# Performance work log

Hardware: AMD Instinct MI355X
Metric: run time of the kernel (lower is better)

Reference implementation:

```python
import jax, jax.numpy as jnp
import numpy as np

NU = 60000   # num_users
NI = 40000   # num_items
N = NU + NI  # num_nodes
E = 2000000  # num_edges
F = 128      # feat_dim (user_feat_dim == item_feat_dim)
H = 128      # hidden_dim


def setup_inputs() -> dict:
    key = jax.random.key(0)
    ks = jax.random.split(key, 14)
    s = 0.05
    inp = {
        "x": jax.random.normal(ks[0], (N, F), jnp.float32),
        "edge_index": jax.random.randint(ks[1], (2, E), 0, N, dtype=jnp.int32),
        "node_type": jnp.concatenate([jnp.zeros(NU, jnp.int32), jnp.ones(NI, jnp.int32)]),
        # input projections (Linear stores weight as (out, in))
        "w_user": s * jax.random.normal(ks[2], (H, F), jnp.float32),
        "b_user": jnp.zeros((H,), jnp.float32),
        "w_item": s * jax.random.normal(ks[3], (H, F), jnp.float32),
        "b_item": jnp.zeros((H,), jnp.float32),
        # SAGEConv layer 0: lin_l (aggregated neighbors, with bias), lin_r (root, no bias)
        "w_l0": s * jax.random.normal(ks[4], (H, H), jnp.float32),
        "b_l0": s * jax.random.normal(ks[5], (H,), jnp.float32),
        "w_r0": s * jax.random.normal(ks[6], (H, H), jnp.float32),
        # SAGEConv layer 1
        "w_l1": s * jax.random.normal(ks[7], (H, H), jnp.float32),
        "b_l1": s * jax.random.normal(ks[8], (H,), jnp.float32),
        "w_r1": s * jax.random.normal(ks[9], (H, H), jnp.float32),
    }
    return inp


def _sage_conv(h, src, dst, w_l, b_l, w_r):
    # gather source features, max-aggregate onto destinations (PyG aggr='max')
    msg = h[src]                                          # [E, H]
    agg = jax.ops.segment_max(msg, dst, num_segments=N)   # [N, H], -inf where no in-edges
    agg = jnp.where(jnp.isneginf(agg), 0.0, agg)          # PyG fills empty segments with 0
    return agg @ w_l.T + b_l + h @ w_r.T


def reference(x, edge_index, node_type, w_user, b_user, w_item, b_item,
              w_l0, b_l0, w_r0, w_l1, b_l1, w_r1):
    # node_type is sorted: first NU rows are users, rest are items
    src, dst = edge_index[0], edge_index[1]
    user_h = x[:NU] @ w_user.T + b_user                   # [NU, H]
    item_h = x[NU:] @ w_item.T + b_item                   # [NI, H]
    h = jnp.concatenate([user_h, item_h], axis=0)         # [N, H]
    # layer 0 with residual (dims match) then ReLU; dropout is identity in eval
    h = h + _sage_conv(h, src, dst, w_l0, b_l0, w_r0)
    h = jax.nn.relu(h)
    # layer 1 with residual (no activation after last layer)
    h = h + _sage_conv(h, src, dst, w_l1, b_l1, w_r1)
    return (h[:NU], h[NU:])
```

## Files before the change

kernel.cpp:

```cpp
#include <hip/hip_runtime.h>

#define NUSR 60000
#define NITM 40000
#define NN   100000
#define EE   2000000
#define HD   128

#define BW   512
#define NB   196
#define EPB  8192

using bf16x8   = __attribute__((ext_vector_type(8))) short;
using f32x4    = __attribute__((ext_vector_type(4))) float;
using ushort4t = __attribute__((ext_vector_type(4))) unsigned short;
using ushort2t = __attribute__((ext_vector_type(2))) unsigned short;
using ushort8t = __attribute__((ext_vector_type(8))) unsigned short;
using uint4t   = __attribute__((ext_vector_type(4))) unsigned int;

__device__ __forceinline__ unsigned short f2bf(float f) {
    unsigned int u = __float_as_uint(f);
    u += 0x7FFFu + ((u >> 16) & 1u);
    return (unsigned short)(u >> 16);
}
__device__ __forceinline__ float bf2f(unsigned short s) {
    return __uint_as_float(((unsigned int)s) << 16);
}
__device__ __forceinline__ unsigned short keyof(unsigned short b) {
    return (b & 0x8000u) ? (unsigned short)~b : (unsigned short)(b | 0x8000u);
}
__device__ __forceinline__ unsigned unkey32(unsigned k) {
    unsigned negsel = (~k & 0x80008000u) >> 15;
    return k ^ (0x80008000u | (negsel * 0x7FFFu));
}
__device__ __forceinline__ int swz(int row, int col) {
    return row * HD + (col ^ ((row & 7) << 3));
}
__device__ __forceinline__ ushort8t pkmax8(ushort8t a, ushort8t b) {
    return __builtin_elementwise_max(a, b);
}

__global__ __launch_bounds__(256) void bhist_k(const int* __restrict__ dst,
                                               int* __restrict__ bcnt) {
    __shared__ int h[NB];
    int t = threadIdx.x;
    if (t < NB) h[t] = 0;
    __syncthreads();
    int e0 = blockIdx.x * EPB;
    #pragma unroll 4
    for (int i = t; i < EPB; i += 256) {
        int e = e0 + i;
        if (e < EE) atomicAdd(&h[dst[e] >> 9], 1);
    }
    __syncthreads();
    if (t < NB && h[t]) atomicAdd(&bcnt[t], h[t]);
}

__global__ void bscan_k(const int* __restrict__ bcnt, int* __restrict__ bbase,
                        int* __restrict__ bcur, int* __restrict__ off) {
    __shared__ int s[256];
    int t = threadIdx.x;
    int v = (t < NB) ? bcnt[t] : 0;
    s[t] = v;
    __syncthreads();
    for (int d = 1; d < 256; d <<= 1) {
        int a = (t >= d) ? s[t - d] : 0;
        __syncthreads();
        s[t] += a;
        __syncthreads();
    }
    if (t < NB) { bbase[t] = s[t] - v; bcur[t] = s[t] - v; }
    if (t == NB - 1) { bbase[NB] = s[t]; off[NN] = EE; }
}

__global__ __launch_bounds__(256) void bscatter_k(const int* __restrict__ src,
                                                  const int* __restrict__ dst,
                                                  int* __restrict__ bcur,
                                                  unsigned int* __restrict__ bedge) {
    __shared__ int h[NB], base[NB];
    int t = threadIdx.x;
    if (t < NB) h[t] = 0;
    __syncthreads();
    int e0 = blockIdx.x * EPB;
    #pragma unroll 4
    for (int i = t; i < EPB; i += 256) {
        int e = e0 + i;
        if (e < EE) atomicAdd(&h[dst[e] >> 9], 1);
    }
    __syncthreads();
    if (t < NB) {
        int c = h[t];
        base[t] = c ? atomicAdd(&bcur[t], c) : 0;
        h[t] = 0;
    }
    __syncthreads();
    #pragma unroll 4
    for (int i = t; i < EPB; i += 256) {
        int e = e0 + i;
        if (e < EE) {
            int d = dst[e];
            int b = d >> 9;
            int p = base[b] + atomicAdd(&h[b], 1);
            bedge[p] = ((unsigned)(d - (b << 9)) << 17) | (unsigned)src[e];
        }
    }
}

__global__ __launch_bounds__(512) void bcsr_k(const unsigned int* __restrict__ bedge,
                                              const int* __restrict__ bbase,
                                              int* __restrict__ off,
                                              int* __restrict__ csr) {
    __shared__ int cnt[BW], cur[BW], sc[BW];
    int b = blockIdx.x, t = threadIdx.x;
    int n0 = b * BW;
    int nloc = min(BW, NN - n0);
    cnt[t] = 0;
    __syncthreads();
    int e0 = bbase[b], e1 = bbase[b + 1];
    for (int e = e0 + t; e < e1; e += 512)
        atomicAdd(&cnt[bedge[e] >> 17], 1);
    __syncthreads();
    int v = cnt[t];
    sc[t] = v;
    __syncthreads();
    for (int d = 1; d < BW; d <<= 1) {
        int a = (t >= d) ? sc[t - d] : 0;
        __syncthreads();
        sc[t] += a;
        __syncthreads();
    }
    int excl = sc[t] - v;
    if (t < nloc) { off[n0 + t] = e0 + excl; cur[t] = e0 + excl; }
    __syncthreads();
    for (int e = e0 + t; e < e1; e += 512) {
        unsigned ed = bedge[e];
        int p = atomicAdd(&cur[ed >> 17], 1);
        csr[p] = (int)(ed & 0x1FFFFu);
    }
}

__global__ void cvt6_k(const float* __restrict__ a0, const float* __restrict__ a1,
                       const float* __restrict__ a2, const float* __restrict__ a3,
                       const float* __restrict__ a4, const float* __restrict__ a5,
                       unsigned short* __restrict__ out) {
    int i = blockIdx.x * 256 + threadIdx.x;
    const float* s;
    switch (i >> 14) {
        case 0: s = a0; break; case 1: s = a1; break; case 2: s = a2; break;
        case 3: s = a3; break; case 4: s = a4; break; default: s = a5; break;
    }
    out[i] = f2bf(s[i & 16383]);
}

__global__ __launch_bounds__(256) void proj_mfma_k(
    const float* __restrict__ x, const unsigned short* __restrict__ wb,
    const float* __restrict__ bias, unsigned short* __restrict__ hkey,
    int row_base, int nrows) {
    __shared__ unsigned short lw[HD * HD];
    int tid = threadIdx.x;
    #pragma unroll
    for (int it = 0; it < 16; ++it) {
        int flat = (it * 256 + tid) * 4;
        int row = flat >> 7, col = flat & 127;
        *(ushort4t*)&lw[swz(row, col)] = *(const ushort4t*)(wb + flat);
    }
    __syncthreads();
    int lane = tid & 63, w = tid >> 6;
    int l15 = lane & 15, l4 = lane >> 4;
    int m0 = blockIdx.x * 128 + w * 32;
    f32x4 acc[2][8] = {};
    #pragma unroll
    for (int kb = 0; kb < 4; ++kb) {
        bf16x8 a[2];
        #pragma unroll
        for (int rt = 0; rt < 2; ++rt) {
            int r = m0 + rt * 16 + l15;
            if (r >= nrows) r = nrows - 1;
            const float* ap = x + (size_t)(row_base + r) * HD + kb * 32 + l4 * 8;
            f32x4 v0 = *(const f32x4*)ap;
            f32x4 v1 = *(const f32x4*)(ap + 4);
            bf16x8 f;
            #pragma unroll
            for (int j = 0; j < 4; ++j) { f[j] = (short)f2bf(v0[j]); f[j + 4] = (short)f2bf(v1[j]); }
            a[rt] = f;
        }
        #pragma unroll
        for (int ct = 0; ct < 8; ++ct) {
            bf16x8 b = *(const bf16x8*)&lw[swz(ct * 16 + l15, kb * 32 + l4 * 8)];
            acc[0][ct] = __builtin_amdgcn_mfma_f32_16x16x32_bf16(a[0], b, acc[0][ct], 0, 0, 0);
            acc[1][ct] = __builtin_amdgcn_mfma_f32_16x16x32_bf16(a[1], b, acc[1][ct], 0, 0, 0);
        }
    }
    __syncthreads();
    #pragma unroll
    for (int ct = 0; ct < 8; ++ct) {
        int col = ct * 16 + l15;
        float bv = bias[col];
        #pragma unroll
        for (int rt = 0; rt < 2; ++rt)
            #pragma unroll
            for (int j = 0; j < 4; ++j) {
                int lrow = w * 32 + rt * 16 + l4 * 4 + j;
                lw[lrow * HD + ((col + ((lrow & 15) << 3)) & 127)] =
                    keyof(f2bf(acc[rt][ct][j] + bv));
            }
    }
    __syncthreads();
    int row = tid >> 1, cb = (tid & 1) * 64;
    int r = blockIdx.x * 128 + row;
    if (r < nrows) {
        int sof = (row & 15) << 3;
        #pragma unroll
        for (int gg = 0; gg < 8; ++gg) {
            uint4t v = *(const uint4t*)&lw[row * HD + ((cb + gg * 8 + sof) & 127)];
            *(uint4t*)(hkey + (size_t)(row_base + r) * HD + cb + gg * 8) = v;
        }
    }
}

__global__ __launch_bounds__(256) void agg_key_k(
    const uint4t* __restrict__ hkey4,
    const int* __restrict__ off, const int* __restrict__ csr,
    uint4t* __restrict__ agg4) {
    int node = (blockIdx.x * 256 + threadIdx.x) >> 6;
    int lane = threadIdx.x & 63;
    if (node >= NN) return;
    int s0 = off[node], s1 = off[node + 1];
    int deg = s1 - s0;
    int q = lane >> 4, l16 = lane & 15;
    ushort8t m = {0, 0, 0, 0, 0, 0, 0, 0};
    int cval = (lane < deg) ? csr[s0 + lane] : 0;
    int nslots = deg < 64 ? deg : 64;
    #pragma unroll
    for (int u = 0; u < 16; ++u) {
        int idx = u * 4 + q;
        int r = __shfl(cval, idx, 64);
        if (idx < nslots) {
            uint4t v = hkey4[(size_t)r * 16 + l16];
            m = pkmax8(m, *(ushort8t*)&v);
        }
    }
    for (int base = s0 + 64; base < s1; base += 32) {
        #pragma unroll
        for (int u = 0; u < 8; ++u) {
            int jj = base + u * 4 + q;
            if (jj < s1) {
                int r = csr[jj];
                uint4t v = hkey4[(size_t)r * 16 + l16];
                m = pkmax8(m, *(ushort8t*)&v);
            }
        }
    }
    uint4t mu = *(uint4t*)&m;
    #pragma unroll
    for (int c = 0; c < 4; ++c) {
        unsigned a = mu[c];
        unsigned b = (unsigned)__shfl_xor((int)a, 16, 64);
        ushort2t pa = *(ushort2t*)&a, pb = *(ushort2t*)&b;
        pa = __builtin_elementwise_max(pa, pb);
        a = *(unsigned*)&pa;
        b = (unsigned)__shfl_xor((int)a, 32, 64);
        pb = *(ushort2t*)&b;
        pa = __builtin_elementwise_max(pa, pb);
        mu[c] = *(unsigned*)&pa;
    }
    if (q == 0) {
        uint4t outv = {0, 0, 0, 0};
        if (deg > 0) {
            #pragma unroll
            for (int c = 0; c < 4; ++c) outv[c] = unkey32(mu[c]);
        }
        agg4[(size_t)node * 16 + l16] = outv;
    }
}

__global__ __launch_bounds__(512) void combine_mfma_k(
    const unsigned short* __restrict__ hkey, const unsigned short* __restrict__ aggb,
    const unsigned short* __restrict__ wlb, const float* __restrict__ bl,
    const unsigned short* __restrict__ wrb,
    unsigned short* __restrict__ hkey_out, float* __restrict__ fout, int relu) {
    __shared__ unsigned short lw[2][HD * HD];
    int tid = threadIdx.x;
    #pragma unroll
    for (int it = 0; it < 8; ++it) {
        int flat = (it * 512 + tid) * 4;
        int row = flat >> 7, col = flat & 127;
        *(ushort4t*)&lw[0][swz(row, col)] = *(const ushort4t*)(wlb + flat);
        *(ushort4t*)&lw[1][swz(row, col)] = *(const ushort4t*)(wrb + flat);
    }
    __syncthreads();
    int lane = tid & 63, w = tid >> 6;
    int l15 = lane & 15, l4 = lane >> 4;
    int m0 = blockIdx.x * 256 + w * 32;
    const uint4t* hk4 = (const uint4t*)hkey;
    f32x4 acc[2][8] = {};
    #pragma unroll
    for (int kb = 0; kb < 4; ++kb) {
        bf16x8 a1[2], a2[2];
        #pragma unroll
        for (int rt = 0; rt < 2; ++rt) {
            int r = m0 + rt * 16 + l15;
            if (r >= NN) r = NN - 1;
            size_t o = (size_t)r * HD + kb * 32 + l4 * 8;
            a1[rt] = *(const bf16x8*)(aggb + o);
            uint4t aw = hk4[(size_t)r * 16 + kb * 4 + l4];
            bf16x8 f;
            #pragma unroll
            for (int u = 0; u < 4; ++u) {
                unsigned d = unkey32(aw[u]);
                f[2 * u]     = (short)(d & 0xFFFFu);
                f[2 * u + 1] = (short)(d >> 16);
            }
            a2[rt] = f;
        }
        #pragma unroll
        for (int ct = 0; ct < 8; ++ct) {
            bf16x8 b1 = *(const bf16x8*)&lw[0][swz(ct * 16 + l15, kb * 32 + l4 * 8)];
            bf16x8 b2 = *(const bf16x8*)&lw[1][swz(ct * 16 + l15, kb * 32 + l4 * 8)];
            acc[0][ct] = __builtin_amdgcn_mfma_f32_16x16x32_bf16(a1[0], b1, acc[0][ct], 0, 0, 0);
            acc[0][ct] = __builtin_amdgcn_mfma_f32_16x16x32_bf16(a2[0], b2, acc[0][ct], 0, 0, 0);
            acc[1][ct] = __builtin_amdgcn_mfma_f32_16x16x32_bf16(a1[1], b1, acc[1][ct], 0, 0, 0);
            acc[1][ct] = __builtin_amdgcn_mfma_f32_16x16x32_bf16(a2[1], b2, acc[1][ct], 0, 0, 0);
        }
    }
    __syncthreads();
    float* cs = (float*)lw;
    for (int p = 0; p < 2; ++p) {
        if ((w >> 2) == p) {
            #pragma unroll
            for (int ct = 0; ct < 8; ++ct)
                #pragma unroll
                for (int rt = 0; rt < 2; ++rt)
                    #pragma unroll
                    for (int j = 0; j < 4; ++j) {
                        int lrow = (w & 3) * 32 + rt * 16 + l4 * 4 + j;
                        int col = ct * 16 + l15;
                        cs[lrow * HD + ((col + lrow * 4) & 127)] = acc[rt][ct][j];
                    }
        }
        __syncthreads();
        int lrow = tid >> 2, cq = (tid & 3) * 32;
        int r = blockIdx.x * 256 + p * 128 + lrow;
        if (r < NN) {
            const float* crow = cs + lrow * HD;
            int rot = lrow * 4;
            #pragma unroll
            for (int gg = 0; gg < 4; ++gg) {
                int c0 = cq + gg * 8;
                uint4t res = *(const uint4t*)(hkey + (size_t)r * HD + c0);
                f32x4 cv0 = *(const f32x4*)&crow[(c0 + rot) & 127];
                f32x4 cv1 = *(const f32x4*)&crow[(c0 + 4 + rot) & 127];
                f32x4 bv0 = *(const f32x4*)(bl + c0);
                f32x4 bv1 = *(const f32x4*)(bl + c0 + 4);
                float v[8];
                #pragma unroll
                for (int u = 0; u < 4; ++u) {
                    unsigned d = unkey32(res[u]);
                    float c_lo = (u < 2) ? cv0[u * 2]     : cv1[(u - 2) * 2];
                    float c_hi = (u < 2) ? cv0[u * 2 + 1] : cv1[(u - 2) * 2 + 1];
                    float b_lo = (u < 2) ? bv0[u * 2]     : bv1[(u - 2) * 2];
                    float b_hi = (u < 2) ? bv0[u * 2 + 1] : bv1[(u - 2) * 2 + 1];
                    v[2 * u]     = c_lo + b_lo + bf2f((unsigned short)(d & 0xFFFFu));
                    v[2 * u + 1] = c_hi + b_hi + bf2f((unsigned short)(d >> 16));
                }
                if (relu) {
                    #pragma unroll
                    for (int u = 0; u < 8; ++u) v[u] = fmaxf(v[u], 0.0f);
                }
                if (fout) {
                    f32x4 o0 = {v[0], v[1], v[2], v[3]};
                    f32x4 o1 = {v[4], v[5], v[6], v[7]};
                    *(f32x4*)(fout + (size_t)r * HD + c0) = o0;
                    *(f32x4*)(fout + (size_t)r * HD + c0 + 4) = o1;
                } else {
                    uint4t ov;
                    #pragma unroll
                    for (int u = 0; u < 4; ++u)
                        ov[u] = (unsigned)keyof(f2bf(v[2 * u]))
                              | ((unsigned)keyof(f2bf(v[2 * u + 1])) << 16);
                    *(uint4t*)(hkey_out + (size_t)r * HD + c0) = ov;
                }
            }
        }
        __syncthreads();
    }
}

extern "C" void kernel_launch(void* const* d_in, const int* in_sizes, int n_in,
                              void* d_out, int out_size, void* d_ws, size_t ws_size,
                              hipStream_t stream) {
    const float* x      = (const float*)d_in[0];
    const int*   ei     = (const int*)d_in[1];
    const float* w_user = (const float*)d_in[3];
    const float* b_user = (const float*)d_in[4];
    const float* w_item = (const float*)d_in[5];
    const float* b_item = (const float*)d_in[6];
    const float* w_l0   = (const float*)d_in[7];
    const float* b_l0   = (const float*)d_in[8];
    const float* w_r0   = (const float*)d_in[9];
    const float* w_l1   = (const float*)d_in[10];
    const float* b_l1   = (const float*)d_in[11];
    const float* w_r1   = (const float*)d_in[12];

    const int* e_src = ei;
    const int* e_dst = ei + EE;

    char* ws = (char*)d_ws;
    size_t cur_off = 0;
    auto carve = [&](size_t bytes) {
        void* p = ws + cur_off;
        cur_off = (cur_off + bytes + 255) & ~(size_t)255;
        return p;
    };
    unsigned short* hkey0 = (unsigned short*)carve((size_t)NN * HD * 2);
    unsigned short* hkey1 = (unsigned short*)carve((size_t)NN * HD * 2);
    unsigned short* aggb  = (unsigned short*)carve((size_t)NN * HD * 2);
    unsigned short* wb    = (unsigned short*)carve((size_t)6 * HD * HD * 2);
    int*      off   = (int*)carve((size_t)(NN + 1) * 4);
    int*      csr   = (int*)carve((size_t)EE * 4);
    unsigned* bedge = (unsigned*)carve((size_t)EE * 4);
    int*      bcnt  = (int*)carve((NB + 1) * 4);
    int*      bbase = (int*)carve((NB + 1) * 4);
    int*      bcur  = (int*)carve((NB + 1) * 4);
    (void)ws_size;

    hipMemsetAsync(bcnt, 0, (size_t)NB * 4, stream);
    int nbB = (EE + EPB - 1) / EPB;
    bhist_k<<<nbB, 256, 0, stream>>>(e_dst, bcnt);
    bscan_k<<<1, 256, 0, stream>>>(bcnt, bbase, bcur, off);
    bscatter_k<<<nbB, 256, 0, stream>>>(e_src, e_dst, bcur, bedge);
    bcsr_k<<<NB, 512, 0, stream>>>(bedge, bbase, off, csr);

    cvt6_k<<<(6 * HD * HD) / 256, 256, 0, stream>>>(w_user, w_item, w_l0, w_r0, w_l1, w_r1, wb);

    proj_mfma_k<<<(NUSR + 127) / 128, 256, 0, stream>>>(x, wb,         b_user, hkey0, 0,    NUSR);
    proj_mfma_k<<<(NITM + 127) / 128, 256, 0, stream>>>(x, wb + 16384, b_item, hkey0, NUSR, NITM);

    agg_key_k<<<NN / 4, 256, 0, stream>>>((const uint4t*)hkey0, off, csr, (uint4t*)aggb);
    combine_mfma_k<<<(NN + 255) / 256, 512, 0, stream>>>(
        hkey0, aggb, wb + 2 * 16384, b_l0, wb + 3 * 16384, hkey1, nullptr, 1);

    agg_key_k<<<NN / 4, 256, 0, stream>>>((const uint4t*)hkey1, off, csr, (uint4t*)aggb);
    combine_mfma_k<<<(NN + 255) / 256, 512, 0, stream>>>(
        hkey1, aggb, wb + 4 * 16384, b_l1, wb + 5 * 16384, nullptr, (float*)d_out, 0);
}
```

Measured before the change: 314.3 us.

## Pre-pack MFMA weight fragments, fold residual into W_r, drop LDS weight staging

```diff
diff --git a/kernel.cpp b/kernel.cpp
--- a/kernel.cpp
+++ b/kernel.cpp
@@ -31,9 +31,6 @@
 __device__ __forceinline__ unsigned unkey32(unsigned k) {
     unsigned negsel = (~k & 0x80008000u) >> 15;
     return k ^ (0x80008000u | (negsel * 0x7FFFu));
-}
-__device__ __forceinline__ int swz(int row, int col) {
-    return row * HD + (col ^ ((row & 7) << 3));
 }
 __device__ __forceinline__ ushort8t pkmax8(ushort8t a, ushort8t b) {
     return __builtin_elementwise_max(a, b);
@@ -138,32 +135,38 @@
     }
 }
 
-__global__ void cvt6_k(const float* __restrict__ a0, const float* __restrict__ a1,
-                       const float* __restrict__ a2, const float* __restrict__ a3,
-                       const float* __restrict__ a4, const float* __restrict__ a5,
-                       unsigned short* __restrict__ out) {
-    int i = blockIdx.x * 256 + threadIdx.x;
+__global__ void pack6_k(const float* __restrict__ a0, const float* __restrict__ a1,
+                        const float* __restrict__ a2, const float* __restrict__ a3,
+                        const float* __restrict__ a4, const float* __restrict__ a5,
+                        unsigned short* __restrict__ wp) {
+    int g = blockIdx.x * 256 + threadIdx.x;
+    int m = g >> 11, rem = g & 2047;
+    int kb = rem >> 9, rem2 = rem & 511;
+    int ct = rem2 >> 6, lane = rem2 & 63;
+    int l15 = lane & 15, l4 = lane >> 4;
     const float* s;
-    switch (i >> 14) {
+    switch (m) {
         case 0: s = a0; break; case 1: s = a1; break; case 2: s = a2; break;
         case 3: s = a3; break; case 4: s = a4; break; default: s = a5; break;
     }
-    out[i] = f2bf(s[i & 16383]);
+    int n = ct * 16 + l15, k0 = kb * 32 + l4 * 8;
+    int addI = (m == 3 || m == 5);
+    ushort8t o;
+    #pragma unroll
+    for (int j = 0; j < 8; ++j) {
+        float v = s[n * HD + k0 + j];
+        if (addI && n == (k0 + j)) v += 1.0f;
+        o[j] = f2bf(v);
+    }
+    *(ushort8t*)&wp[(size_t)g * 8] = o;
 }
 
 __global__ __launch_bounds__(256) void proj_mfma_k(
-    const float* __restrict__ x, const unsigned short* __restrict__ wb,
+    const float* __restrict__ x, const unsigned short* __restrict__ wpk,
     const float* __restrict__ bias, unsigned short* __restrict__ hkey,
     int row_base, int nrows) {
-    __shared__ unsigned short lw[HD * HD];
+    __shared__ unsigned short lk[HD * HD];
     int tid = threadIdx.x;
-    #pragma unroll
-    for (int it = 0; it < 16; ++it) {
-        int flat = (it * 256 + tid) * 4;
-        int row = flat >> 7, col = flat & 127;
-        *(ushort4t*)&lw[swz(row, col)] = *(const ushort4t*)(wb + flat);
-    }
-    __syncthreads();
     int lane = tid & 63, w = tid >> 6;
     int l15 = lane & 15, l4 = lane >> 4;
     int m0 = blockIdx.x * 128 + w * 32;
@@ -185,12 +188,11 @@
         }
         #pragma unroll
         for (int ct = 0; ct < 8; ++ct) {
-            bf16x8 b = *(const bf16x8*)&lw[swz(ct * 16 + l15, kb * 32 + l4 * 8)];
+            bf16x8 b = *(const bf16x8*)(wpk + (size_t)((kb * 8 + ct) * 64 + lane) * 8);
             acc[0][ct] = __builtin_amdgcn_mfma_f32_16x16x32_bf16(a[0], b, acc[0][ct], 0, 0, 0);
             acc[1][ct] = __builtin_amdgcn_mfma_f32_16x16x32_bf16(a[1], b, acc[1][ct], 0, 0, 0);
         }
     }
-    __syncthreads();
     #pragma unroll
     for (int ct = 0; ct < 8; ++ct) {
         int col = ct * 16 + l15;
@@ -200,7 +202,7 @@
             #pragma unroll
             for (int j = 0; j < 4; ++j) {
                 int lrow = w * 32 + rt * 16 + l4 * 4 + j;
-                lw[lrow * HD + ((col + ((lrow & 15) << 3)) & 127)] =
+                lk[lrow * HD + ((col + ((lrow & 15) << 3)) & 127)] =
                     keyof(f2bf(acc[rt][ct][j] + bv));
             }
     }
@@ -211,7 +213,7 @@
         int sof = (row & 15) << 3;
         #pragma unroll
         for (int gg = 0; gg < 8; ++gg) {
-            uint4t v = *(const uint4t*)&lw[row * HD + ((cb + gg * 8 + sof) & 127)];
+            uint4t v = *(const uint4t*)&lk[row * HD + ((cb + gg * 8 + sof) & 127)];
             *(uint4t*)(hkey + (size_t)(row_base + r) * HD + cb + gg * 8) = v;
         }
     }
@@ -230,8 +232,8 @@
     ushort8t m = {0, 0, 0, 0, 0, 0, 0, 0};
     int cval = (lane < deg) ? csr[s0 + lane] : 0;
     int nslots = deg < 64 ? deg : 64;
-    #pragma unroll
-    for (int u = 0; u < 16; ++u) {
+    int niter = (nslots + 3) >> 2;
+    for (int u = 0; u < niter; ++u) {
         int idx = u * 4 + q;
         int r = __shfl(cval, idx, 64);
         if (idx < nslots) {
@@ -273,24 +275,16 @@
     }
 }
 
-__global__ __launch_bounds__(512) void combine_mfma_k(
+__global__ __launch_bounds__(256) void combine_mfma_k(
     const unsigned short* __restrict__ hkey, const unsigned short* __restrict__ aggb,
-    const unsigned short* __restrict__ wlb, const float* __restrict__ bl,
-    const unsigned short* __restrict__ wrb,
+    const unsigned short* __restrict__ wpk_l, const float* __restrict__ bl,
+    const unsigned short* __restrict__ wpk_r,
     unsigned short* __restrict__ hkey_out, float* __restrict__ fout, int relu) {
-    __shared__ unsigned short lw[2][HD * HD];
+    __shared__ float cs[64 * HD];
     int tid = threadIdx.x;
-    #pragma unroll
-    for (int it = 0; it < 8; ++it) {
-        int flat = (it * 512 + tid) * 4;
-        int row = flat >> 7, col = flat & 127;
-        *(ushort4t*)&lw[0][swz(row, col)] = *(const ushort4t*)(wlb + flat);
-        *(ushort4t*)&lw[1][swz(row, col)] = *(const ushort4t*)(wrb + flat);
-    }
-    __syncthreads();
     int lane = tid & 63, w = tid >> 6;
     int l15 = lane & 15, l4 = lane >> 4;
-    int m0 = blockIdx.x * 256 + w * 32;
+    int m0 = blockIdx.x * 128 + w * 32;
     const uint4t* hk4 = (const uint4t*)hkey;
     f32x4 acc[2][8] = {};
     #pragma unroll
@@ -314,54 +308,44 @@
         }
         #pragma unroll
         for (int ct = 0; ct < 8; ++ct) {
-            bf16x8 b1 = *(const bf16x8*)&lw[0][swz(ct * 16 + l15, kb * 32 + l4 * 8)];
-            bf16x8 b2 = *(const bf16x8*)&lw[1][swz(ct * 16 + l15, kb * 32 + l4 * 8)];
+            size_t fo = (size_t)((kb * 8 + ct) * 64 + lane) * 8;
+            bf16x8 b1 = *(const bf16x8*)(wpk_l + fo);
+            bf16x8 b2 = *(const bf16x8*)(wpk_r + fo);
             acc[0][ct] = __builtin_amdgcn_mfma_f32_16x16x32_bf16(a1[0], b1, acc[0][ct], 0, 0, 0);
             acc[0][ct] = __builtin_amdgcn_mfma_f32_16x16x32_bf16(a2[0], b2, acc[0][ct], 0, 0, 0);
             acc[1][ct] = __builtin_amdgcn_mfma_f32_16x16x32_bf16(a1[1], b1, acc[1][ct], 0, 0, 0);
             acc[1][ct] = __builtin_amdgcn_mfma_f32_16x16x32_bf16(a2[1], b2, acc[1][ct], 0, 0, 0);
         }
     }
-    __syncthreads();
-    float* cs = (float*)lw;
     for (int p = 0; p < 2; ++p) {
-        if ((w >> 2) == p) {
+        if ((w >> 1) == p) {
             #pragma unroll
             for (int ct = 0; ct < 8; ++ct)
                 #pragma unroll
                 for (int rt = 0; rt < 2; ++rt)
                     #pragma unroll
                     for (int j = 0; j < 4; ++j) {
-                        int lrow = (w & 3) * 32 + rt * 16 + l4 * 4 + j;
+                        int lrow = (w & 1) * 32 + rt * 16 + l4 * 4 + j;
                         int col = ct * 16 + l15;
                         cs[lrow * HD + ((col + lrow * 4) & 127)] = acc[rt][ct][j];
                     }
         }
         __syncthreads();
         int lrow = tid >> 2, cq = (tid & 3) * 32;
-        int r = blockIdx.x * 256 + p * 128 + lrow;
+        int r = blockIdx.x * 128 + p * 64 + lrow;
         if (r < NN) {
             const float* crow = cs + lrow * HD;
             int rot = lrow * 4;
             #pragma unroll
             for (int gg = 0; gg < 4; ++gg) {
                 int c0 = cq + gg * 8;
-                uint4t res = *(const uint4t*)(hkey + (size_t)r * HD + c0);
                 f32x4 cv0 = *(const f32x4*)&crow[(c0 + rot) & 127];
                 f32x4 cv1 = *(const f32x4*)&crow[(c0 + 4 + rot) & 127];
                 f32x4 bv0 = *(const f32x4*)(bl + c0);
                 f32x4 bv1 = *(const f32x4*)(bl + c0 + 4);
                 float v[8];
                 #pragma unroll
-                for (int u = 0; u < 4; ++u) {
-                    unsigned d = unkey32(res[u]);
-                    float c_lo = (u < 2) ? cv0[u * 2]     : cv1[(u - 2) * 2];
-                    float c_hi = (u < 2) ? cv0[u * 2 + 1] : cv1[(u - 2) * 2 + 1];
-                    float b_lo = (u < 2) ? bv0[u * 2]     : bv1[(u - 2) * 2];
-                    float b_hi = (u < 2) ? bv0[u * 2 + 1] : bv1[(u - 2) * 2 + 1];
-                    v[2 * u]     = c_lo + b_lo + bf2f((unsigned short)(d & 0xFFFFu));
-                    v[2 * u + 1] = c_hi + b_hi + bf2f((unsigned short)(d >> 16));
-                }
+                for (int u = 0; u < 4; ++u) { v[u] = cv0[u] + bv0[u]; v[u + 4] = cv1[u] + bv1[u]; }
                 if (relu) {
                     #pragma unroll
                     for (int u = 0; u < 8; ++u) v[u] = fmaxf(v[u], 0.0f);
@@ -414,7 +398,7 @@
     unsigned short* hkey0 = (unsigned short*)carve((size_t)NN * HD * 2);
     unsigned short* hkey1 = (unsigned short*)carve((size_t)NN * HD * 2);
     unsigned short* aggb  = (unsigned short*)carve((size_t)NN * HD * 2);
-    unsigned short* wb    = (unsigned short*)carve((size_t)6 * HD * HD * 2);
+    unsigned short* wpk   = (unsigned short*)carve((size_t)6 * HD * HD * 2);
     int*      off   = (int*)carve((size_t)(NN + 1) * 4);
     int*      csr   = (int*)carve((size_t)EE * 4);
     unsigned* bedge = (unsigned*)carve((size_t)EE * 4);
@@ -430,16 +414,16 @@
     bscatter_k<<<nbB, 256, 0, stream>>>(e_src, e_dst, bcur, bedge);
     bcsr_k<<<NB, 512, 0, stream>>>(bedge, bbase, off, csr);
 
-    cvt6_k<<<(6 * HD * HD) / 256, 256, 0, stream>>>(w_user, w_item, w_l0, w_r0, w_l1, w_r1, wb);
-
-    proj_mfma_k<<<(NUSR + 127) / 128, 256, 0, stream>>>(x, wb,         b_user, hkey0, 0,    NUSR);
-    proj_mfma_k<<<(NITM + 127) / 128, 256, 0, stream>>>(x, wb + 16384, b_item, hkey0, NUSR, NITM);
+    pack6_k<<<48, 256, 0, stream>>>(w_user, w_item, w_l0, w_r0, w_l1, w_r1, wpk);
+
+    proj_mfma_k<<<(NUSR + 127) / 128, 256, 0, stream>>>(x, wpk,         b_user, hkey0, 0,    NUSR);
+    proj_mfma_k<<<(NITM + 127) / 128, 256, 0, stream>>>(x, wpk + 16384, b_item, hkey0, NUSR, NITM);
 
     agg_key_k<<<NN / 4, 256, 0, stream>>>((const uint4t*)hkey0, off, csr, (uint4t*)aggb);
-    combine_mfma_k<<<(NN + 255) / 256, 512, 0, stream>>>(
-        hkey0, aggb, wb + 2 * 16384, b_l0, wb + 3 * 16384, hkey1, nullptr, 1);
+    combine_mfma_k<<<(NN + 127) / 128, 256, 0, stream>>>(
+        hkey0, aggb, wpk + 2 * 16384, b_l0, wpk + 3 * 16384, hkey1, nullptr, 1);
 
     agg_key_k<<<NN / 4, 256, 0, stream>>>((const uint4t*)hkey1, off, csr, (uint4t*)aggb);
-    combine_mfma_k<<<(NN + 255) / 256, 512, 0, stream>>>(
-        hkey1, aggb, wb + 4 * 16384, b_l1, wb + 5 * 16384, nullptr, (float*)d_out, 0);
-}
+    combine_mfma_k<<<(NN + 127) / 128, 256, 0, stream>>>(
+        hkey1, aggb, wpk + 4 * 16384, b_l1, wpk + 5 * 16384, nullptr, (float*)d_out, 0);
+}
```

Result: slower. 333.3 us (+6.0%).

## Slice max-aggregation by feature columns and fold residual into identity weight

Applied to the files above, without the earlier changes.

```diff
diff --git a/kernel.cpp b/kernel.cpp
--- a/kernel.cpp
+++ b/kernel.cpp
@@ -9,12 +9,12 @@
 #define BW   512
 #define NB   196
 #define EPB  8192
+#define NPB  128
 
 using bf16x8   = __attribute__((ext_vector_type(8))) short;
 using f32x4    = __attribute__((ext_vector_type(4))) float;
 using ushort4t = __attribute__((ext_vector_type(4))) unsigned short;
 using ushort2t = __attribute__((ext_vector_type(2))) unsigned short;
-using ushort8t = __attribute__((ext_vector_type(8))) unsigned short;
 using uint4t   = __attribute__((ext_vector_type(4))) unsigned int;
 
 __device__ __forceinline__ unsigned short f2bf(float f) {
@@ -34,9 +34,6 @@
 }
 __device__ __forceinline__ int swz(int row, int col) {
     return row * HD + (col ^ ((row & 7) << 3));
-}
-__device__ __forceinline__ ushort8t pkmax8(ushort8t a, ushort8t b) {
-    return __builtin_elementwise_max(a, b);
 }
 
 __global__ __launch_bounds__(256) void bhist_k(const int* __restrict__ dst,
@@ -138,17 +135,20 @@
     }
 }
 
-__global__ void cvt6_k(const float* __restrict__ a0, const float* __restrict__ a1,
-                       const float* __restrict__ a2, const float* __restrict__ a3,
-                       const float* __restrict__ a4, const float* __restrict__ a5,
-                       unsigned short* __restrict__ out) {
+__global__ void cvt6i_k(const float* __restrict__ a0, const float* __restrict__ a1,
+                        const float* __restrict__ a2, const float* __restrict__ a3,
+                        const float* __restrict__ a4, const float* __restrict__ a5,
+                        unsigned short* __restrict__ out) {
     int i = blockIdx.x * 256 + threadIdx.x;
+    int m = i >> 14, idx = i & 16383;
     const float* s;
-    switch (i >> 14) {
+    switch (m) {
         case 0: s = a0; break; case 1: s = a1; break; case 2: s = a2; break;
         case 3: s = a3; break; case 4: s = a4; break; default: s = a5; break;
     }
-    out[i] = f2bf(s[i & 16383]);
+    float v = s[idx];
+    if ((m == 3 || m == 5) && (idx >> 7) == (idx & 127)) v += 1.0f;
+    out[i] = f2bf(v);
 }
 
 __global__ __launch_bounds__(256) void proj_mfma_k(
@@ -217,64 +217,41 @@
     }
 }
 
-__global__ __launch_bounds__(256) void agg_key_k(
-    const uint4t* __restrict__ hkey4,
+__global__ __launch_bounds__(256) void agg_slice_k(
+    const unsigned* __restrict__ hk32,
     const int* __restrict__ off, const int* __restrict__ csr,
-    uint4t* __restrict__ agg4) {
-    int node = (blockIdx.x * 256 + threadIdx.x) >> 6;
-    int lane = threadIdx.x & 63;
-    if (node >= NN) return;
-    int s0 = off[node], s1 = off[node + 1];
-    int deg = s1 - s0;
-    int q = lane >> 4, l16 = lane & 15;
-    ushort8t m = {0, 0, 0, 0, 0, 0, 0, 0};
-    int cval = (lane < deg) ? csr[s0 + lane] : 0;
-    int nslots = deg < 64 ? deg : 64;
-    #pragma unroll
-    for (int u = 0; u < 16; ++u) {
-        int idx = u * 4 + q;
-        int r = __shfl(cval, idx, 64);
-        if (idx < nslots) {
-            uint4t v = hkey4[(size_t)r * 16 + l16];
-            m = pkmax8(m, *(ushort8t*)&v);
-        }
-    }
-    for (int base = s0 + 64; base < s1; base += 32) {
-        #pragma unroll
-        for (int u = 0; u < 8; ++u) {
-            int jj = base + u * 4 + q;
-            if (jj < s1) {
-                int r = csr[jj];
-                uint4t v = hkey4[(size_t)r * 16 + l16];
-                m = pkmax8(m, *(ushort8t*)&v);
-            }
-        }
-    }
-    uint4t mu = *(uint4t*)&m;
-    #pragma unroll
-    for (int c = 0; c < 4; ++c) {
-        unsigned a = mu[c];
-        unsigned b = (unsigned)__shfl_xor((int)a, 16, 64);
-        ushort2t pa = *(ushort2t*)&a, pb = *(ushort2t*)&b;
-        pa = __builtin_elementwise_max(pa, pb);
-        a = *(unsigned*)&pa;
-        b = (unsigned)__shfl_xor((int)a, 32, 64);
-        pb = *(ushort2t*)&b;
-        pa = __builtin_elementwise_max(pa, pb);
-        mu[c] = *(unsigned*)&pa;
-    }
-    if (q == 0) {
-        uint4t outv = {0, 0, 0, 0};
-        if (deg > 0) {
-            #pragma unroll
-            for (int c = 0; c < 4; ++c) outv[c] = unkey32(mu[c]);
-        }
-        agg4[(size_t)node * 16 + l16] = outv;
+    unsigned* __restrict__ aggS32) {
+    int b = blockIdx.x;
+    int slice = b & 7;
+    int n0 = (b >> 3) * NPB;
+    int n1 = min(n0 + NPB, NN);
+    int wv = threadIdx.x >> 6, lane = threadIdx.x & 63;
+    int oct = lane >> 3, d = lane & 7;
+    unsigned sb = slice * 8 + d;
+    for (int n = n0 + wv; n < n1; n += 4) {
+        int s0 = off[n], s1 = off[n + 1];
+        ushort2t m = {0, 0};
+        for (int j = s0 + oct; j < s1; j += 8) {
+            int r = csr[j];
+            unsigned v = hk32[(size_t)r * 64 + sb];
+            m = __builtin_elementwise_max(m, *(ushort2t*)&v);
+        }
+        unsigned a = *(unsigned*)&m;
+        #pragma unroll
+        for (int x = 8; x < 64; x <<= 1) {
+            unsigned o = (unsigned)__shfl_xor((int)a, x, 64);
+            ushort2t pa = *(ushort2t*)&a, pb = *(ushort2t*)&o;
+            pa = __builtin_elementwise_max(pa, pb);
+            a = *(unsigned*)&pa;
+        }
+        if (oct == 0)
+            aggS32[(size_t)slice * NN * 8 + (size_t)n * 8 + d] =
+                (s1 > s0) ? unkey32(a) : 0u;
     }
 }
 
 __global__ __launch_bounds__(512) void combine_mfma_k(
-    const unsigned short* __restrict__ hkey, const unsigned short* __restrict__ aggb,
+    const unsigned short* __restrict__ hkey, const unsigned short* __restrict__ aggS,
     const unsigned short* __restrict__ wlb, const float* __restrict__ bl,
     const unsigned short* __restrict__ wrb,
     unsigned short* __restrict__ hkey_out, float* __restrict__ fout, int relu) {
@@ -296,12 +273,12 @@
     #pragma unroll
     for (int kb = 0; kb < 4; ++kb) {
         bf16x8 a1[2], a2[2];
+        int sl = kb * 2 + (l4 >> 1);
         #pragma unroll
         for (int rt = 0; rt < 2; ++rt) {
             int r = m0 + rt * 16 + l15;
             if (r >= NN) r = NN - 1;
-            size_t o = (size_t)r * HD + kb * 32 + l4 * 8;
-            a1[rt] = *(const bf16x8*)(aggb + o);
+            a1[rt] = *(const bf16x8*)(aggS + ((size_t)sl * NN + r) * 16 + (l4 & 1) * 8);
             uint4t aw = hk4[(size_t)r * 16 + kb * 4 + l4];
             bf16x8 f;
             #pragma unroll
@@ -346,22 +323,13 @@
             #pragma unroll
             for (int gg = 0; gg < 4; ++gg) {
                 int c0 = cq + gg * 8;
-                uint4t res = *(const uint4t*)(hkey + (size_t)r * HD + c0);
                 f32x4 cv0 = *(const f32x4*)&crow[(c0 + rot) & 127];
                 f32x4 cv1 = *(const f32x4*)&crow[(c0 + 4 + rot) & 127];
                 f32x4 bv0 = *(const f32x4*)(bl + c0);
                 f32x4 bv1 = *(const f32x4*)(bl + c0 + 4);
                 float v[8];
                 #pragma unroll
-                for (int u = 0; u < 4; ++u) {
-                    unsigned d = unkey32(res[u]);
-                    float c_lo = (u < 2) ? cv0[u * 2]     : cv1[(u - 2) * 2];
-                    float c_hi = (u < 2) ? cv0[u * 2 + 1] : cv1[(u - 2) * 2 + 1];
-                    float b_lo = (u < 2) ? bv0[u * 2]     : bv1[(u - 2) * 2];
-                    float b_hi = (u < 2) ? bv0[u * 2 + 1] : bv1[(u - 2) * 2 + 1];
-                    v[2 * u]     = c_lo + b_lo + bf2f((unsigned short)(d & 0xFFFFu));
-                    v[2 * u + 1] = c_hi + b_hi + bf2f((unsigned short)(d >> 16));
-                }
+                for (int u = 0; u < 4; ++u) { v[u] = cv0[u] + bv0[u]; v[u + 4] = cv1[u] + bv1[u]; }
                 if (relu) {
                     #pragma unroll
                     for (int u = 0; u < 8; ++u) v[u] = fmaxf(v[u], 0.0f);
@@ -413,7 +381,7 @@
     };
     unsigned short* hkey0 = (unsigned short*)carve((size_t)NN * HD * 2);
     unsigned short* hkey1 = (unsigned short*)carve((size_t)NN * HD * 2);
-    unsigned short* aggb  = (unsigned short*)carve((size_t)NN * HD * 2);
+    unsigned short* aggS  = (unsigned short*)carve((size_t)NN * HD * 2);
     unsigned short* wb    = (unsigned short*)carve((size_t)6 * HD * HD * 2);
     int*      off   = (int*)carve((size_t)(NN + 1) * 4);
     int*      csr   = (int*)carve((size_t)EE * 4);
@@ -430,16 +398,17 @@
     bscatter_k<<<nbB, 256, 0, stream>>>(e_src, e_dst, bcur, bedge);
     bcsr_k<<<NB, 512, 0, stream>>>(bedge, bbase, off, csr);
 
-    cvt6_k<<<(6 * HD * HD) / 256, 256, 0, stream>>>(w_user, w_item, w_l0, w_r0, w_l1, w_r1, wb);
+    cvt6i_k<<<(6 * HD * HD) / 256, 256, 0, stream>>>(w_user, w_item, w_l0, w_r0, w_l1, w_r1, wb);
 
     proj_mfma_k<<<(NUSR + 127) / 128, 256, 0, stream>>>(x, wb,         b_user, hkey0, 0,    NUSR);
     proj_mfma_k<<<(NITM + 127) / 128, 256, 0, stream>>>(x, wb + 16384, b_item, hkey0, NUSR, NITM);
 
-    agg_key_k<<<NN / 4, 256, 0, stream>>>((const uint4t*)hkey0, off, csr, (uint4t*)aggb);
+    int aggGrid = ((NN + NPB - 1) / NPB) * 8;
+    agg_slice_k<<<aggGrid, 256, 0, stream>>>((const unsigned*)hkey0, off, csr, (unsigned*)aggS);
     combine_mfma_k<<<(NN + 255) / 256, 512, 0, stream>>>(
-        hkey0, aggb, wb + 2 * 16384, b_l0, wb + 3 * 16384, hkey1, nullptr, 1);
-
-    agg_key_k<<<NN / 4, 256, 0, stream>>>((const uint4t*)hkey1, off, csr, (uint4t*)aggb);
+        hkey0, aggS, wb + 2 * 16384, b_l0, wb + 3 * 16384, hkey1, nullptr, 1);
+
+    agg_slice_k<<<aggGrid, 256, 0, stream>>>((const unsigned*)hkey1, off, csr, (unsigned*)aggS);
     combine_mfma_k<<<(NN + 255) / 256, 512, 0, stream>>>(
-        hkey1, aggb, wb + 4 * 16384, b_l1, wb + 5 * 16384, nullptr, (float*)d_out, 0);
-}
+        hkey1, aggS, wb + 4 * 16384, b_l1, wb + 5 * 16384, nullptr, (float*)d_out, 0);
+}
```

Result: slower. 763.7 us (+142.9%).
